# Kernel optimization log

Hardware: AMD Instinct MI355X
Metric: run time of the kernel (lower is better)

Reference implementation:

```python
import jax, jax.numpy as jnp
import numpy as np
from jax import lax

B, C_IN, L = 512, 32, 512
E = 8
POOL = 16            # AdaptiveAvgPool1d(16)
D_IN = C_IN * L      # expert input = flattened x
D_OUT = 768          # pooler_output dim (hard-coded in module)
TAU = 1.0            # gumbel temperature
BN_EPS = 1e-5


def setup_inputs() -> dict:
    key = jax.random.key(0)
    ks = jax.random.split(key, 8)
    s = 0.02
    return {
        "x": jax.random.normal(ks[0], (B, C_IN, L), jnp.float32),
        "gumbel_u": jax.random.uniform(ks[1], (B, E), jnp.float32, 1e-6, 1.0 - 1e-6),
        "conv_w": jax.random.normal(ks[2], (64, C_IN, 3), jnp.float32) * s,
        "conv_b": jnp.zeros((64,), jnp.float32),
        "bn_gamma": jnp.ones((64 * POOL,), jnp.float32),
        "bn_beta": jnp.zeros((64 * POOL,), jnp.float32),
        "bn_mean": jnp.zeros((64 * POOL,), jnp.float32),
        "bn_var": jnp.ones((64 * POOL,), jnp.float32),
        "fc1_w": jax.random.normal(ks[3], (128, 64 * POOL), jnp.float32) * s,
        "fc1_b": jnp.zeros((128,), jnp.float32),
        "fc2_w": jax.random.normal(ks[4], (E, 128), jnp.float32) * s,
        "fc2_b": jnp.zeros((E,), jnp.float32),
        "expert_w": jax.random.normal(ks[5], (E, D_IN, D_OUT), jnp.float32) * s,
        "expert_b": jnp.zeros((E, D_OUT), jnp.float32),
    }


def _gelu(v):
    return jax.nn.gelu(v, approximate=False)  # torch nn.GELU default (erf)


def reference(x, gumbel_u, conv_w, conv_b, bn_gamma, bn_beta, bn_mean, bn_var,
              fc1_w, fc1_b, fc2_w, fc2_b, expert_w, expert_b):
    # ---- router ----
    h = lax.conv_general_dilated(x, conv_w, (1,), ((1, 1),),
                                 dimension_numbers=("NCH", "OIH", "NCH"))
    h = _gelu(h + conv_b[None, :, None])                     # [B,64,L]
    h = h.reshape(B, 64, POOL, L // POOL).mean(-1)           # adaptive avg pool -> [B,64,16]
    h = h.reshape(B, 64 * POOL)                              # flatten
    h = (h - bn_mean) * lax.rsqrt(bn_var + BN_EPS) * bn_gamma + bn_beta  # BN (eval)
    h = _gelu(h @ fc1_w.T + fc1_b)                           # dropout inactive in eval
    logits = h @ fc2_w.T + fc2_b                             # [B,E]

    # ---- soft gumbel-softmax gating (hard=False), then top-2 ----
    g = -jnp.log(-jnp.log(gumbel_u))
    routing_weights = jax.nn.softmax((logits + g) / TAU, axis=1)
    topv, topi = lax.top_k(routing_weights, 2)               # [B,2]
    w = topv / (topv.sum(axis=1, keepdims=True) + 1e-8)      # [B,2]

    # ---- dispatch/compute/combine (dense-expert stand-in: flatten + linear) ----
    xf = x.reshape(B, D_IN)
    all_out = jnp.einsum("bd,edh->beh", xf, expert_w) + expert_b[None]  # [B,E,768]
    sel = jnp.take_along_axis(all_out, topi[:, :, None], axis=1)        # [B,2,768]
    pooler_output = (sel * w[:, :, None]).sum(axis=1)                   # [B,768]
    return pooler_output
```

## Files before the change

### kernel.cpp

```cpp
#include <hip/hip_runtime.h>
#include <hip/hip_bf16.h>

#define NB 512
#define CIN 32
#define LEN 512
#define NE 8
#define NPOOL 16
#define DIN 16384
#define DOUT 768
#define HD 1024
#define F1 128

#define MT 256
#define NT 128
#define BK 32
#define NBUF 4

typedef __attribute__((ext_vector_type(4))) float f32x4;
typedef __attribute__((ext_vector_type(8))) short s16x8;
typedef __attribute__((ext_vector_type(4))) unsigned int u32x4;

__device__ __forceinline__ float gelu_erf(float v) {
    return 0.5f * v * (1.0f + erff(v * 0.70710678118654752f));
}

__device__ __forceinline__ unsigned cvt_pk(float lo, float hi) {
    unsigned r;
    asm volatile("v_cvt_pk_bf16_f32 %0, %1, %2" : "=v"(r) : "v"(lo), "v"(hi));
    return r;
}

__device__ __forceinline__ unsigned short f2bf_u(float f) {
    union { float f; unsigned u; } x; x.f = f;
    unsigned r = x.u + 0x7fffu + ((x.u >> 16) & 1u);
    return (unsigned short)(r >> 16);
}

__device__ __forceinline__ void gload_lds16(const void* gptr, void* lptr) {
    __builtin_amdgcn_global_load_lds(
        (const __attribute__((address_space(1))) unsigned int*)gptr,
        (__attribute__((address_space(3))) unsigned int*)lptr,
        16, 0, 0);
}

__global__ __launch_bounds__(256) void kcvt(const float* __restrict__ x,
                                            unsigned short* __restrict__ xb)
{
    int i = blockIdx.x * 256 + threadIdx.x;
    const f32x4* src = (const f32x4*)(x + (size_t)i * 8);
    f32x4 v0 = src[0], v1 = src[1];
    u32x4 pk;
    pk[0] = cvt_pk(v0[0], v0[1]); pk[1] = cvt_pk(v0[2], v0[3]);
    pk[2] = cvt_pk(v1[0], v1[1]); pk[3] = cvt_pk(v1[2], v1[3]);
    *(u32x4*)(xb + (size_t)i * 8) = pk;
}

__global__ __launch_bounds__(256) void krouter_conv(
    const float* __restrict__ x, const float* __restrict__ cw, const float* __restrict__ cb,
    const float* __restrict__ bng, const float* __restrict__ bnb,
    const float* __restrict__ bnm, const float* __restrict__ bnv,
    float* __restrict__ h, int* __restrict__ cnt)
{
    __shared__ float xs[CIN * 264];
    int half = blockIdx.x;
    int b = blockIdx.y;
    int t = threadIdx.x;
    if (b == 0 && half == 0 && t < NE) cnt[t] = 0;

    int Lchunk0 = half * 64 - 1;
    const float* xb_ = x + (size_t)b * DIN;
    for (int idx = t; idx < CIN * 66; idx += 256) {
        int ci = idx / 66;
        int cc = idx - ci * 66;
        int gc = min(max(Lchunk0 + cc, 0), 127);
        f32x4 v = *(const f32x4*)(xb_ + ci * 512 + gc * 4);
        int byte = ci * 1056 + ((cc << 4) ^ (((cc >> 3) & 7) << 4));
        *(f32x4*)((char*)xs + byte) = v;
    }
    __syncthreads();

    int p  = t & 7;
    int pg = half * 8 + p;
    int cq = t >> 3;
    int co0 = cq * 2, co1 = co0 + 1;

    float sa[32], sb[32];
    #pragma unroll
    for (int i = 0; i < 32; ++i) { sa[i] = 0.f; sb[i] = 0.f; }

    for (int ci = 0; ci < CIN; ++ci) {
        float f[40];
        #pragma unroll
        for (int u = 0; u < 10; ++u) {
            int lc = p * 8 + u;
            int byte = ci * 1056 + ((lc << 4) ^ (((lc >> 3) & 7) << 4));
            f32x4 v = *(const f32x4*)((const char*)xs + byte);
            f[4*u+0] = v[0]; f[4*u+1] = v[1]; f[4*u+2] = v[2]; f[4*u+3] = v[3];
        }
        if (pg == 0)  f[3]  = 0.f;
        if (pg == 15) f[36] = 0.f;
        float wa0 = cw[co0*96 + ci*3 + 0], wa1 = cw[co0*96 + ci*3 + 1], wa2 = cw[co0*96 + ci*3 + 2];
        float wb0 = cw[co1*96 + ci*3 + 0], wb1 = cw[co1*96 + ci*3 + 1], wb2 = cw[co1*96 + ci*3 + 2];
        #pragma unroll
        for (int i = 0; i < 32; ++i) {
            sa[i] = fmaf(f[i+3], wa0, fmaf(f[i+4], wa1, fmaf(f[i+5], wa2, sa[i])));
            sb[i] = fmaf(f[i+3], wb0, fmaf(f[i+4], wb1, fmaf(f[i+5], wb2, sb[i])));
        }
    }

    float ba = cb[co0], bbv = cb[co1];
    float ma = 0.f, mb = 0.f;
    #pragma unroll
    for (int i = 0; i < 32; ++i) { ma += gelu_erf(sa[i] + ba); mb += gelu_erf(sb[i] + bbv); }
    ma *= (1.f / 32.f); mb *= (1.f / 32.f);

    int oa = co0 * NPOOL + pg, ob = co1 * NPOOL + pg;
    float ra = (ma - bnm[oa]) * rsqrtf(bnv[oa] + 1e-5f) * bng[oa] + bnb[oa];
    float rb = (mb - bnm[ob]) * rsqrtf(bnv[ob] + 1e-5f) * bng[ob] + bnb[ob];
    h[(size_t)b * HD + oa] = ra;
    h[(size_t)b * HD + ob] = rb;
}

__global__ __launch_bounds__(256) void krouter_fc(
    const float* __restrict__ h, const float* __restrict__ f1w, const float* __restrict__ f1b,
    const float* __restrict__ f2w, const float* __restrict__ f2b,
    const float* __restrict__ gu,
    int* __restrict__ top2e, float* __restrict__ top2w,
    int* __restrict__ cnt, int* __restrict__ rowlist, float* __restrict__ roww)
{
    __shared__ float hs[8 * HD];
    __shared__ float h1s[8 * F1];
    __shared__ float lg[8 * NE];

    int bb = blockIdx.x * 8;
    int t = threadIdx.x;

    const f32x4* hg = (const f32x4*)(h + (size_t)bb * HD);
    f32x4* hs4 = (f32x4*)hs;
    #pragma unroll
    for (int u = 0; u < 8; ++u) hs4[t + 256 * u] = hg[t + 256 * u];
    __syncthreads();

    int j = t & 127;
    int pr = t >> 7;
    float acc[4] = {0.f, 0.f, 0.f, 0.f};
    const f32x4* w4 = (const f32x4*)(f1w + (size_t)j * HD);
    for (int k4 = 0; k4 < 256; ++k4) {
        f32x4 w = w4[k4];
        #pragma unroll
        for (int g = 0; g < 4; ++g) {
            f32x4 hv = hs4[(pr * 4 + g) * 256 + k4];
            acc[g] += w[0]*hv[0] + w[1]*hv[1] + w[2]*hv[2] + w[3]*hv[3];
        }
    }
    float bj = f1b[j];
    #pragma unroll
    for (int g = 0; g < 4; ++g) h1s[(pr * 4 + g) * F1 + j] = gelu_erf(acc[g] + bj);
    __syncthreads();

    if (t < 64) {
        int bi = t >> 3, e = t & 7;
        float s = f2b[e];
        const float* w = f2w + e * F1;
        const float* hh = h1s + bi * F1;
        #pragma unroll 8
        for (int k = 0; k < F1; ++k) s += hh[k] * w[k];
        lg[bi * NE + e] = s;
    }
    __syncthreads();

    if (t < 8) {
        int bi = t; int b = bb + bi;
        float r[NE];
        float mx = -1e30f;
        #pragma unroll
        for (int e = 0; e < NE; ++e) {
            float g = -logf(-logf(gu[b * NE + e]));
            r[e] = lg[bi * NE + e] + g;
            mx = fmaxf(mx, r[e]);
        }
        float sum = 0.f;
        #pragma unroll
        for (int e = 0; e < NE; ++e) { r[e] = expf(r[e] - mx); sum += r[e]; }
        float inv = 1.f / sum;
        #pragma unroll
        for (int e = 0; e < NE; ++e) r[e] *= inv;
        int e0 = 0; float v0 = r[0];
        #pragma unroll
        for (int e = 1; e < NE; ++e) if (r[e] > v0) { v0 = r[e]; e0 = e; }
        int e1 = -1; float v1 = -1.f;
        #pragma unroll
        for (int e = 0; e < NE; ++e) { if (e == e0) continue; if (r[e] > v1) { v1 = r[e]; e1 = e; } }
        float den = v0 + v1 + 1e-8f;
        float w0 = v0 / den, w1 = v1 / den;
        top2e[b * 2 + 0] = e0; top2e[b * 2 + 1] = e1;
        top2w[b * 2 + 0] = w0; top2w[b * 2 + 1] = w1;
        int p0 = atomicAdd(&cnt[e0], 1);
        rowlist[e0 * NB + p0] = b * 2 + 0; roww[e0 * NB + p0] = w0;
        int p1 = atomicAdd(&cnt[e1], 1);
        rowlist[e1 * NB + p1] = b * 2 + 1; roww[e1 * NB + p1] = w1;
    }
}

__global__ __launch_bounds__(512, 2) void kgemm(
    const unsigned short* __restrict__ xb, const float* __restrict__ ew,
    const int* __restrict__ cnt, const int* __restrict__ rowlist, const float* __restrict__ roww,
    unsigned short* __restrict__ ypart, int nkc, int kch)
{
    int nwg = gridDim.x;
    int cpx = nwg >> 3;
    int wg = (blockIdx.x & 7) * cpx + (blockIdx.x >> 3);
    int nt = wg % 6;
    int kc = (wg / 6) % nkc;
    int e  = wg / (6 * nkc);
    int cn = cnt[e];
    if (cn <= 0) return;

    __shared__ __align__(16) char As[NBUF][MT * 64];
    __shared__ __align__(16) char Bs[NBUF][BK * NT * 4];

    int t = threadIdx.x;
    int wid = t >> 6, lane = t & 63;
    int wm = wid >> 1, wn = wid & 1;
    int g = lane >> 4;
    int NS = kch / BK;
    int k0 = kc * kch;

    const char* gB = (const char*)ew + (size_t)e * DIN * DOUT * 4
                   + (size_t)k0 * (DOUT * 4) + nt * NT * 4;
    int keyb = wid >> 1;
    int brow0 = wid * 4 + (lane >> 5);
    const char* gpB0 = gB + (size_t)brow0 * (DOUT * 4) + ((size_t)((lane & 31) ^ keyb) << 4);
    const char* gpB1 = gpB0 + 2 * (DOUT * 4);
    int ldsB0 = wid * 2048, ldsB1 = wid * 2048 + 1024;

    int keya = ((lane >> 2) ^ (lane >> 4)) & 3;
    int aq = (lane & 3) ^ keya;
    int ldsA0 = wid * 2048, ldsA1 = wid * 2048 + 1024;

    int af_off[4];
    #pragma unroll
    for (int mi = 0; mi < 4; ++mi) {
        int m = wm * 64 + mi * 16 + (lane & 15);
        int key = ((m & 3) ^ ((m >> 2) & 3));
        af_off[mi] = m * 64 + ((g ^ key) << 4);
    }
    int cb[4];
    #pragma unroll
    for (int ni = 0; ni < 4; ++ni) {
        int n = wn * 64 + ni * 16 + (lane & 15);
        cb[ni] = (((n >> 2) ^ g) << 4) + ((n & 3) << 2);
    }

    for (int row0 = 0; row0 < cn; row0 += MT) {
        int mloc = min(MT, cn - row0);
        bool wact = (wm * 64 < mloc);

        int r0 = wid * 32 + (lane >> 2);
        int r1 = r0 + 16;
        size_t ab0 = (size_t)(rowlist[e * NB + row0 + min(r0, mloc - 1)] >> 1) * (DIN * 2);
        size_t ab1 = (size_t)(rowlist[e * NB + row0 + min(r1, mloc - 1)] >> 1) * (DIN * 2);
        const char* gpA0 = (const char*)xb + ab0 + (size_t)k0 * 2 + (aq << 4);
        const char* gpA1 = (const char*)xb + ab1 + (size_t)k0 * 2 + (aq << 4);

        f32x4 acc[4][4];
        #pragma unroll
        for (int i = 0; i < 4; ++i)
            #pragma unroll
            for (int jj = 0; jj < 4; ++jj) acc[i][jj] = (f32x4){0.f, 0.f, 0.f, 0.f};

        auto stage = [&](int s) {
            int bi = s & (NBUF - 1);
            size_t bo = (size_t)s * (BK * DOUT * 4);
            gload_lds16(gpB0 + bo, (char*)Bs[bi] + ldsB0);
            gload_lds16(gpB1 + bo, (char*)Bs[bi] + ldsB1);
            size_t ao = (size_t)s * (BK * 2);
            gload_lds16(gpA0 + ao, (char*)As[bi] + ldsA0);
            gload_lds16(gpA1 + ao, (char*)As[bi] + ldsA1);
        };

        stage(0);
        if (1 < NS) stage(1);

        for (int s = 0; s < NS; ++s) {
            if (s + 2 < NS) stage(s + 2);
            __builtin_amdgcn_sched_barrier(0);
            if (s + 2 < NS)      asm volatile("s_waitcnt vmcnt(8)" ::: "memory");
            else if (s + 1 < NS) asm volatile("s_waitcnt vmcnt(4)" ::: "memory");
            else                 asm volatile("s_waitcnt vmcnt(0)" ::: "memory");
            __builtin_amdgcn_sched_barrier(0);
            __builtin_amdgcn_s_barrier();
            __builtin_amdgcn_sched_barrier(0);

            if (wact) {
                const char* Ab = As[s & (NBUF - 1)];
                const char* Bb = Bs[s & (NBUF - 1)];
                __builtin_amdgcn_s_setprio(1);
                s16x8 af[4];
                #pragma unroll
                for (int mi = 0; mi < 4; ++mi)
                    af[mi] = *(const s16x8*)(Ab + af_off[mi]);
                #pragma unroll
                for (int ni = 0; ni < 4; ++ni) {
                    float v[8];
                    #pragma unroll
                    for (int j = 0; j < 8; ++j)
                        v[j] = *(const float*)(Bb + g * 4096 + j * 512 + cb[ni]);
                    union { u32x4 u; s16x8 v8; } bf;
                    bf.u[0] = cvt_pk(v[0], v[1]); bf.u[1] = cvt_pk(v[2], v[3]);
                    bf.u[2] = cvt_pk(v[4], v[5]); bf.u[3] = cvt_pk(v[6], v[7]);
                    #pragma unroll
                    for (int mi = 0; mi < 4; ++mi)
                        acc[mi][ni] = __builtin_amdgcn_mfma_f32_16x16x32_bf16(af[mi], bf.v8, acc[mi][ni], 0, 0, 0);
                }
                __builtin_amdgcn_s_setprio(0);
            }
        }

        if (wact) {
            #pragma unroll
            for (int mi = 0; mi < 4; ++mi) {
                #pragma unroll
                for (int rg = 0; rg < 4; ++rg) {
                    int m = wm * 64 + mi * 16 + g * 4 + rg;
                    if (m < mloc) {
                        int ent = rowlist[e * NB + row0 + m];
                        float wgt = roww[e * NB + row0 + m];
                        int ob = ent >> 1, slot = ent & 1;
                        unsigned short* dst = ypart + ((size_t)(slot * nkc + kc) * NB + ob) * DOUT
                                            + nt * NT + wn * 64 + (lane & 15);
                        #pragma unroll
                        for (int ni = 0; ni < 4; ++ni)
                            dst[ni * 16] = f2bf_u(acc[mi][ni][rg] * wgt);
                    }
                }
            }
        }
        asm volatile("s_waitcnt vmcnt(0) lgkmcnt(0)" ::: "memory");
        __builtin_amdgcn_s_barrier();
    }
}

__global__ __launch_bounds__(256) void kcombine(
    const unsigned short* __restrict__ ypart,
    const int* __restrict__ top2e, const float* __restrict__ top2w,
    const float* __restrict__ eb, float* __restrict__ out, int nplanes)
{
    int b = blockIdx.y;
    int n = blockIdx.x * 256 + threadIdx.x;
    float s = 0.f;
    for (int p = 0; p < nplanes; ++p) {
        unsigned v = ypart[((size_t)p * NB + b) * DOUT + n];
        union { unsigned u; float f; } c; c.u = v << 16;
        s += c.f;
    }
    int e0 = top2e[b * 2], e1 = top2e[b * 2 + 1];
    float w0 = top2w[b * 2], w1 = top2w[b * 2 + 1];
    s += w0 * eb[e0 * DOUT + n] + w1 * eb[e1 * DOUT + n];
    out[(size_t)b * DOUT + n] = s;
}

extern "C" void kernel_launch(void* const* d_in, const int* in_sizes, int n_in,
                              void* d_out, int out_size, void* d_ws, size_t ws_size,
                              hipStream_t stream)
{
    const float* x   = (const float*)d_in[0];
    const float* gu  = (const float*)d_in[1];
    const float* cw  = (const float*)d_in[2];
    const float* cb  = (const float*)d_in[3];
    const float* bng = (const float*)d_in[4];
    const float* bnb = (const float*)d_in[5];
    const float* bnm = (const float*)d_in[6];
    const float* bnv = (const float*)d_in[7];
    const float* f1w = (const float*)d_in[8];
    const float* f1b = (const float*)d_in[9];
    const float* f2w = (const float*)d_in[10];
    const float* f2b = (const float*)d_in[11];
    const float* ew  = (const float*)d_in[12];
    const float* eb  = (const float*)d_in[13];

    int nkc = (ws_size >= (size_t)48 * 1024 * 1024) ? 16 : 8;
    int kch = DIN / nkc;

    char* ws = (char*)d_ws;
    size_t off = 0;
    float* h       = (float*)(ws + off); off += (size_t)NB * HD * 4;
    int*   top2e   = (int*)(ws + off);   off += (size_t)NB * 2 * 4;
    float* top2w   = (float*)(ws + off); off += (size_t)NB * 2 * 4;
    int*   cnt     = (int*)(ws + off);   off += 256;
    int*   rowlist = (int*)(ws + off);   off += (size_t)NE * NB * 4;
    float* roww    = (float*)(ws + off); off += (size_t)NE * NB * 4;
    unsigned short* xbuf = (unsigned short*)(ws + off);
    off += (size_t)NB * DIN * 2;
    unsigned short* ypart = (unsigned short*)(ws + off);
    off += (size_t)2 * nkc * NB * DOUT * 2;

    kcvt<<<NB * DIN / 8 / 256, 256, 0, stream>>>(x, xbuf);
    krouter_conv<<<dim3(2, NB), 256, 0, stream>>>(x, cw, cb, bng, bnb, bnm, bnv, h, cnt);
    krouter_fc<<<NB / 8, 256, 0, stream>>>(h, f1w, f1b, f2w, f2b, gu,
                                           top2e, top2w, cnt, rowlist, roww);
    kgemm<<<NE * nkc * 6, 512, 0, stream>>>(xbuf, ew, cnt, rowlist, roww, ypart, nkc, kch);
    kcombine<<<dim3(3, NB), 256, 0, stream>>>(ypart, top2e, top2w, eb, (float*)d_out, 2 * nkc);
}
```

Before: 253.4 us.

## Fuse bf16 cast into router conv, halve fc block, warp-specialize GEMM

Drops the separate x-to-bf16 kernel and writes the bf16 copy from the conv kernel's tile load, saving one full pass over x. The router FC kernel now handles 4 rows per block instead of 8, doubling its grid. The expert GEMM becomes warp-specialized: 4 producer waves stage B through registers and A with global_load_lds into a double-buffered BK=64 LDS tile, while 8 consumer waves run the MFMAs. The old 4-deep async pipeline with fine-grained vmcnt waits is replaced by a __syncthreads per stage, which may expose more memory latency. The launch bound also moves to 768 threads with 3 blocks requested per SM.

```diff
diff --git a/kernel.cpp b/kernel.cpp
--- a/kernel.cpp
+++ b/kernel.cpp
@@ -13,8 +13,7 @@
 
 #define MT 256
 #define NT 128
-#define BK 32
-#define NBUF 4
+#define BK 64
 
 typedef __attribute__((ext_vector_type(4))) float f32x4;
 typedef __attribute__((ext_vector_type(8))) short s16x8;
@@ -43,23 +42,11 @@
         16, 0, 0);
 }
 
-__global__ __launch_bounds__(256) void kcvt(const float* __restrict__ x,
-                                            unsigned short* __restrict__ xb)
-{
-    int i = blockIdx.x * 256 + threadIdx.x;
-    const f32x4* src = (const f32x4*)(x + (size_t)i * 8);
-    f32x4 v0 = src[0], v1 = src[1];
-    u32x4 pk;
-    pk[0] = cvt_pk(v0[0], v0[1]); pk[1] = cvt_pk(v0[2], v0[3]);
-    pk[2] = cvt_pk(v1[0], v1[1]); pk[3] = cvt_pk(v1[2], v1[3]);
-    *(u32x4*)(xb + (size_t)i * 8) = pk;
-}
-
 __global__ __launch_bounds__(256) void krouter_conv(
     const float* __restrict__ x, const float* __restrict__ cw, const float* __restrict__ cb,
     const float* __restrict__ bng, const float* __restrict__ bnb,
     const float* __restrict__ bnm, const float* __restrict__ bnv,
-    float* __restrict__ h, int* __restrict__ cnt)
+    float* __restrict__ h, int* __restrict__ cnt, unsigned short* __restrict__ xbuf)
 {
     __shared__ float xs[CIN * 264];
     int half = blockIdx.x;
@@ -76,6 +63,14 @@
         f32x4 v = *(const f32x4*)(xb_ + ci * 512 + gc * 4);
         int byte = ci * 1056 + ((cc << 4) ^ (((cc >> 3) & 7) << 4));
         *(f32x4*)((char*)xs + byte) = v;
+        if (cc >= 1 && cc <= 64) {
+            int gc2 = Lchunk0 + cc;
+            unsigned lo = cvt_pk(v[0], v[1]);
+            unsigned hi = cvt_pk(v[2], v[3]);
+            unsigned long long pk8 = ((unsigned long long)hi << 32) | lo;
+            *(unsigned long long*)((char*)xbuf
+                + ((size_t)b * DIN + ci * 512 + gc2 * 4) * 2) = pk8;
+        }
     }
     __syncthreads();
 
@@ -128,37 +123,37 @@
     int* __restrict__ top2e, float* __restrict__ top2w,
     int* __restrict__ cnt, int* __restrict__ rowlist, float* __restrict__ roww)
 {
-    __shared__ float hs[8 * HD];
-    __shared__ float h1s[8 * F1];
-    __shared__ float lg[8 * NE];
-
-    int bb = blockIdx.x * 8;
+    __shared__ float hs[4 * HD];
+    __shared__ float h1s[4 * F1];
+    __shared__ float lg[4 * NE];
+
+    int bb = blockIdx.x * 4;
     int t = threadIdx.x;
 
     const f32x4* hg = (const f32x4*)(h + (size_t)bb * HD);
     f32x4* hs4 = (f32x4*)hs;
     #pragma unroll
-    for (int u = 0; u < 8; ++u) hs4[t + 256 * u] = hg[t + 256 * u];
+    for (int u = 0; u < 4; ++u) hs4[t + 256 * u] = hg[t + 256 * u];
     __syncthreads();
 
     int j = t & 127;
     int pr = t >> 7;
-    float acc[4] = {0.f, 0.f, 0.f, 0.f};
+    float acc[2] = {0.f, 0.f};
     const f32x4* w4 = (const f32x4*)(f1w + (size_t)j * HD);
     for (int k4 = 0; k4 < 256; ++k4) {
         f32x4 w = w4[k4];
         #pragma unroll
-        for (int g = 0; g < 4; ++g) {
-            f32x4 hv = hs4[(pr * 4 + g) * 256 + k4];
+        for (int g = 0; g < 2; ++g) {
+            f32x4 hv = hs4[(pr * 2 + g) * 256 + k4];
             acc[g] += w[0]*hv[0] + w[1]*hv[1] + w[2]*hv[2] + w[3]*hv[3];
         }
     }
     float bj = f1b[j];
     #pragma unroll
-    for (int g = 0; g < 4; ++g) h1s[(pr * 4 + g) * F1 + j] = gelu_erf(acc[g] + bj);
+    for (int g = 0; g < 2; ++g) h1s[(pr * 2 + g) * F1 + j] = gelu_erf(acc[g] + bj);
     __syncthreads();
 
-    if (t < 64) {
+    if (t < 32) {
         int bi = t >> 3, e = t & 7;
         float s = f2b[e];
         const float* w = f2w + e * F1;
@@ -169,7 +164,7 @@
     }
     __syncthreads();
 
-    if (t < 8) {
+    if (t < 4) {
         int bi = t; int b = bb + bi;
         float r[NE];
         float mx = -1e30f;
@@ -202,7 +197,7 @@
     }
 }
 
-__global__ __launch_bounds__(512, 2) void kgemm(
+__global__ __launch_bounds__(768, 3) void kgemm(
     const unsigned short* __restrict__ xb, const float* __restrict__ ew,
     const int* __restrict__ cnt, const int* __restrict__ rowlist, const float* __restrict__ roww,
     unsigned short* __restrict__ ypart, int nkc, int kch)
@@ -216,52 +211,52 @@
     int cn = cnt[e];
     if (cn <= 0) return;
 
-    __shared__ __align__(16) char As[NBUF][MT * 64];
-    __shared__ __align__(16) char Bs[NBUF][BK * NT * 4];
+    __shared__ __align__(16) char Al[2][MT * 128];
+    __shared__ __align__(16) char Bl[2][BK * 512];
 
     int t = threadIdx.x;
     int wid = t >> 6, lane = t & 63;
-    int wm = wid >> 1, wn = wid & 1;
-    int g = lane >> 4;
     int NS = kch / BK;
     int k0 = kc * kch;
-
-    const char* gB = (const char*)ew + (size_t)e * DIN * DOUT * 4
-                   + (size_t)k0 * (DOUT * 4) + nt * NT * 4;
-    int keyb = wid >> 1;
-    int brow0 = wid * 4 + (lane >> 5);
-    const char* gpB0 = gB + (size_t)brow0 * (DOUT * 4) + ((size_t)((lane & 31) ^ keyb) << 4);
-    const char* gpB1 = gpB0 + 2 * (DOUT * 4);
-    int ldsB0 = wid * 2048, ldsB1 = wid * 2048 + 1024;
-
-    int keya = ((lane >> 2) ^ (lane >> 4)) & 3;
-    int aq = (lane & 3) ^ keya;
-    int ldsA0 = wid * 2048, ldsA1 = wid * 2048 + 1024;
-
-    int af_off[4];
-    #pragma unroll
-    for (int mi = 0; mi < 4; ++mi) {
-        int m = wm * 64 + mi * 16 + (lane & 15);
-        int key = ((m & 3) ^ ((m >> 2) & 3));
-        af_off[mi] = m * 64 + ((g ^ key) << 4);
-    }
-    int cb[4];
-    #pragma unroll
-    for (int ni = 0; ni < 4; ++ni) {
-        int n = wn * 64 + ni * 16 + (lane & 15);
-        cb[ni] = (((n >> 2) ^ g) << 4) + ((n & 3) << 2);
-    }
+    bool producer = (wid < 4);
+
+    const char* ewE = (const char*)ew + (size_t)e * DIN * DOUT * 4 + (size_t)nt * NT * 4;
+    const char* bsrc0 = ewE + (size_t)(k0 + wid * 16 + (lane >> 2)) * (DOUT * 4)
+                      + (size_t)(lane & 3) * 16;
+    int bdst_row = (wid * 16 + (lane >> 2)) * 512 + (lane & 3) * 16;
+    int asrc_off = (((lane & 7) ^ ((lane >> 3) & 7)) << 4);
+
+    int cw_ = wid - 4;
+    int wm = cw_ >> 1, wn = cw_ & 1;
+    int g = lane >> 4;
+    int af_off[4][2];
+    #pragma unroll
+    for (int mi = 0; mi < 4; ++mi)
+        #pragma unroll
+        for (int kk = 0; kk < 2; ++kk) {
+            int m = wm * 64 + mi * 16 + (lane & 15);
+            af_off[mi][kk] = m * 128 + (((g + kk * 4) ^ (m & 7)) << 4);
+        }
+    int bn_off[4];
+    #pragma unroll
+    for (int ni = 0; ni < 4; ++ni)
+        bn_off[ni] = (wn * 64 + ni * 16 + (lane & 15)) * 4;
 
     for (int row0 = 0; row0 < cn; row0 += MT) {
         int mloc = min(MT, cn - row0);
-        bool wact = (wm * 64 < mloc);
-
-        int r0 = wid * 32 + (lane >> 2);
-        int r1 = r0 + 16;
-        size_t ab0 = (size_t)(rowlist[e * NB + row0 + min(r0, mloc - 1)] >> 1) * (DIN * 2);
-        size_t ab1 = (size_t)(rowlist[e * NB + row0 + min(r1, mloc - 1)] >> 1) * (DIN * 2);
-        const char* gpA0 = (const char*)xb + ab0 + (size_t)k0 * 2 + (aq << 4);
-        const char* gpA1 = (const char*)xb + ab1 + (size_t)k0 * 2 + (aq << 4);
+
+        const char* abase[8];
+        if (producer) {
+            #pragma unroll
+            for (int jj = 0; jj < 8; ++jj) {
+                int r = (wid * 8 + jj) * 8 + (lane >> 3);
+                int rc = min(row0 + r, cn - 1);
+                int row = rowlist[e * NB + rc] >> 1;
+                abase[jj] = (const char*)xb + (size_t)row * (DIN * 2)
+                          + (size_t)k0 * 2 + asrc_off;
+            }
+        }
+        bool wact = !producer && (wm * 64 < mloc);
 
         f32x4 acc[4][4];
         #pragma unroll
@@ -269,53 +264,58 @@
             #pragma unroll
             for (int jj = 0; jj < 4; ++jj) acc[i][jj] = (f32x4){0.f, 0.f, 0.f, 0.f};
 
-        auto stage = [&](int s) {
-            int bi = s & (NBUF - 1);
-            size_t bo = (size_t)s * (BK * DOUT * 4);
-            gload_lds16(gpB0 + bo, (char*)Bs[bi] + ldsB0);
-            gload_lds16(gpB1 + bo, (char*)Bs[bi] + ldsB1);
-            size_t ao = (size_t)s * (BK * 2);
-            gload_lds16(gpA0 + ao, (char*)As[bi] + ldsA0);
-            gload_lds16(gpA1 + ao, (char*)As[bi] + ldsA1);
-        };
-
-        stage(0);
-        if (1 < NS) stage(1);
+#define STAGE(s_, buf_) {                                                     \
+        const char* bs_ = bsrc0 + (size_t)(s_) * ((size_t)BK * DOUT * 4);     \
+        f32x4 bv[8];                                                          \
+        _Pragma("unroll")                                                     \
+        for (int i = 0; i < 8; ++i)                                           \
+            bv[i] = *(const f32x4*)(bs_ + i * 64);                            \
+        _Pragma("unroll")                                                     \
+        for (int i = 0; i < 8; ++i)                                           \
+            *(f32x4*)(Bl[buf_] + bdst_row + i * 64) = bv[i];                  \
+        size_t ao_ = (size_t)(s_) * (BK * 2);                                 \
+        _Pragma("unroll")                                                     \
+        for (int jj = 0; jj < 8; ++jj)                                        \
+            gload_lds16(abase[jj] + ao_, (char*)Al[buf_] + (wid * 8 + jj) * 1024); }
+
+        if (producer) STAGE(0, 0);
+        __syncthreads();
 
         for (int s = 0; s < NS; ++s) {
-            if (s + 2 < NS) stage(s + 2);
-            __builtin_amdgcn_sched_barrier(0);
-            if (s + 2 < NS)      asm volatile("s_waitcnt vmcnt(8)" ::: "memory");
-            else if (s + 1 < NS) asm volatile("s_waitcnt vmcnt(4)" ::: "memory");
-            else                 asm volatile("s_waitcnt vmcnt(0)" ::: "memory");
-            __builtin_amdgcn_sched_barrier(0);
-            __builtin_amdgcn_s_barrier();
-            __builtin_amdgcn_sched_barrier(0);
-
-            if (wact) {
-                const char* Ab = As[s & (NBUF - 1)];
-                const char* Bb = Bs[s & (NBUF - 1)];
+            int buf = s & 1;
+            if (producer) {
+                if (s + 1 < NS) STAGE(s + 1, buf ^ 1);
+            } else if (wact) {
+                const char* Ab = Al[buf];
+                const char* Bb = Bl[buf];
                 __builtin_amdgcn_s_setprio(1);
-                s16x8 af[4];
                 #pragma unroll
-                for (int mi = 0; mi < 4; ++mi)
-                    af[mi] = *(const s16x8*)(Ab + af_off[mi]);
-                #pragma unroll
-                for (int ni = 0; ni < 4; ++ni) {
-                    float v[8];
-                    #pragma unroll
-                    for (int j = 0; j < 8; ++j)
-                        v[j] = *(const float*)(Bb + g * 4096 + j * 512 + cb[ni]);
-                    union { u32x4 u; s16x8 v8; } bf;
-                    bf.u[0] = cvt_pk(v[0], v[1]); bf.u[1] = cvt_pk(v[2], v[3]);
-                    bf.u[2] = cvt_pk(v[4], v[5]); bf.u[3] = cvt_pk(v[6], v[7]);
+                for (int kk = 0; kk < 2; ++kk) {
+                    s16x8 af[4];
                     #pragma unroll
                     for (int mi = 0; mi < 4; ++mi)
-                        acc[mi][ni] = __builtin_amdgcn_mfma_f32_16x16x32_bf16(af[mi], bf.v8, acc[mi][ni], 0, 0, 0);
+                        af[mi] = *(const s16x8*)(Ab + af_off[mi][kk]);
+                    #pragma unroll
+                    for (int ni = 0; ni < 4; ++ni) {
+                        const char* bp = Bb + (kk * 32 + g * 8) * 512 + bn_off[ni];
+                        float v[8];
+                        #pragma unroll
+                        for (int j = 0; j < 8; ++j)
+                            v[j] = *(const float*)(bp + j * 512);
+                        union { u32x4 u; s16x8 v8; } bf;
+                        bf.u[0] = cvt_pk(v[0], v[1]); bf.u[1] = cvt_pk(v[2], v[3]);
+                        bf.u[2] = cvt_pk(v[4], v[5]); bf.u[3] = cvt_pk(v[6], v[7]);
+                        #pragma unroll
+                        for (int mi = 0; mi < 4; ++mi)
+                            acc[mi][ni] = __builtin_amdgcn_mfma_f32_16x16x32_bf16(
+                                af[mi], bf.v8, acc[mi][ni], 0, 0, 0);
+                    }
                 }
                 __builtin_amdgcn_s_setprio(0);
             }
-        }
+            __syncthreads();
+        }
+#undef STAGE
 
         if (wact) {
             #pragma unroll
@@ -336,8 +336,7 @@
                 }
             }
         }
-        asm volatile("s_waitcnt vmcnt(0) lgkmcnt(0)" ::: "memory");
-        __builtin_amdgcn_s_barrier();
+        __syncthreads();
     }
 }
 
@@ -395,10 +394,9 @@
     unsigned short* ypart = (unsigned short*)(ws + off);
     off += (size_t)2 * nkc * NB * DOUT * 2;
 
-    kcvt<<<NB * DIN / 8 / 256, 256, 0, stream>>>(x, xbuf);
-    krouter_conv<<<dim3(2, NB), 256, 0, stream>>>(x, cw, cb, bng, bnb, bnm, bnv, h, cnt);
-    krouter_fc<<<NB / 8, 256, 0, stream>>>(h, f1w, f1b, f2w, f2b, gu,
+    krouter_conv<<<dim3(2, NB), 256, 0, stream>>>(x, cw, cb, bng, bnb, bnm, bnv, h, cnt, xbuf);
+    krouter_fc<<<NB / 4, 256, 0, stream>>>(h, f1w, f1b, f2w, f2b, gu,
                                            top2e, top2w, cnt, rowlist, roww);
-    kgemm<<<NE * nkc * 6, 512, 0, stream>>>(xbuf, ew, cnt, rowlist, roww, ypart, nkc, kch);
+    kgemm<<<NE * nkc * 6, 768, 0, stream>>>(xbuf, ew, cnt, rowlist, roww, ypart, nkc, kch);
     kcombine<<<dim3(3, NB), 256, 0, stream>>>(ypart, top2e, top2w, eb, (float*)d_out, 2 * nkc);
 }
```

Result: faster. 235.7 us (-7.0%).
